# Performance work log

Measured on AMD Instinct MI355X. Metric: run time of the kernel, lower is better.

## Reference

```python
import jax, jax.numpy as jnp
import numpy as np

B, S, D, H = 4, 2048, 1024, 16
HD = D // H
EPS = 1e-5


def setup_inputs() -> dict:
    key = jax.random.key(0)
    ks = jax.random.split(key, 12)
    scale = 1.0 / np.sqrt(D)
    inp = {
        "x": jax.random.normal(ks[0], (B, S, D), dtype=jnp.float32),
        "template_ids": jax.random.randint(ks[1], (B, S), 0, 1000, dtype=jnp.int64)
            if jax.config.jax_enable_x64 else jax.random.randint(ks[1], (B, S), 0, 1000, dtype=jnp.int32),
        "attention_mask": jnp.ones((B, S), dtype=jnp.int32),
        "Wq": jax.random.normal(ks[2], (D, D), dtype=jnp.float32) * scale,
        "bq": jnp.zeros((D,), dtype=jnp.float32),
        "Wk": jax.random.normal(ks[3], (D, D), dtype=jnp.float32) * scale,
        "bk": jnp.zeros((D,), dtype=jnp.float32),
        "Wv": jax.random.normal(ks[4], (D, D), dtype=jnp.float32) * scale,
        "bv": jnp.zeros((D,), dtype=jnp.float32),
        "Wo": jax.random.normal(ks[5], (D, D), dtype=jnp.float32) * scale,
        "bo": jnp.zeros((D,), dtype=jnp.float32),
        "gamma": jnp.ones((D,), dtype=jnp.float32),
        "beta": jnp.zeros((D,), dtype=jnp.float32),
    }
    return inp


def _split_heads(t):
    # [B,S,D] -> [B,H,S,HD]
    return t.reshape(B, S, H, HD).transpose(0, 2, 1, 3)


def reference(x, template_ids, attention_mask, Wq, bq, Wk, bk, Wv, bv, Wo, bo, gamma, beta):
    q = _split_heads(x @ Wq.T + bq)
    k = _split_heads(x @ Wk.T + bk)
    v = _split_heads(x @ Wv.T + bv)
    # [B,H,S,S]
    scores = jnp.einsum("bhqd,bhkd->bhqk", q, k) / jnp.sqrt(jnp.float32(HD))
    mask = attention_mask[:, None, None, :]  # broadcast over heads and query dim
    scores = jnp.where(mask == 0, jnp.float32(-10000.0), scores)
    attn = jax.nn.softmax(scores, axis=-1)  # dropout is identity in eval
    out = jnp.einsum("bhqk,bhkd->bhqd", attn, v)
    out = out.transpose(0, 2, 1, 3).reshape(B, S, D)
    out = out @ Wo.T + bo
    # residual + LayerNorm
    y = x + out
    mu = jnp.mean(y, axis=-1, keepdims=True)
    var = jnp.var(y, axis=-1, keepdims=True)
    return (y - mu) * jax.lax.rsqrt(var + EPS) * gamma + beta
```

## Files before the change

### kernel.cpp

```cpp
#include <hip/hip_runtime.h>

typedef unsigned short u16;
typedef unsigned int u32;
typedef __attribute__((ext_vector_type(8))) short bf16x8;
typedef __attribute__((ext_vector_type(4))) float f32x4;

#define NB 4
#define SS 2048
#define DD 1024
#define NH 16
#define HD 64
#define MM (NB*SS)

struct __align__(16) Pack16 { unsigned int w0, w1, w2, w3; };
union PU { Pack16 p; u16 s[8]; };

__device__ __forceinline__ float b2f(u16 u) {
    union { unsigned int i; float f; } v; v.i = ((unsigned int)u) << 16; return v.f;
}
__device__ __forceinline__ u16 f2b(float f) {
    union { unsigned int i; float f; } v; v.f = f;
    return (u16)((v.i + 0x7FFFu + ((v.i >> 16) & 1u)) >> 16);
}
__device__ __forceinline__ float rdS(const void* p, size_t i, int mode) {
    return mode ? ((const float*)p)[i] : b2f(((const u16*)p)[i]);
}
__device__ __forceinline__ float ex2(float x) { return __builtin_amdgcn_exp2f(x); }
__device__ __forceinline__ u32 cvtpk(float lo, float hi) {
    u32 r;
    asm("v_cvt_pk_bf16_f32 %0, %1, %2" : "=v"(r) : "v"(lo), "v"(hi));
    return r;
}

__device__ __forceinline__ void cp16(const u16* g, u16* l) {
    __builtin_amdgcn_global_load_lds(
        (const __attribute__((address_space(1))) void*)g,
        (__attribute__((address_space(3))) void*)l, 16, 0, 0);
}

__device__ __forceinline__ void pl32swap(u32& a, u32& b) {
    asm volatile("v_permlane32_swap_b32 %0, %1" : "+v"(a), "+v"(b));
}
__device__ __forceinline__ void pl16swap(u32& a, u32& b) {
    asm volatile("v_permlane16_swap_b32 %0, %1" : "+v"(a), "+v"(b));
}

#define QSC 0.1803368801111204f
#define GX ((size_t)MM * DD / 8)
#define GW ((size_t)DD * DD / 8)
#define GTOT (GX + 4 * GW + 512)

__global__ __launch_bounds__(256) void convert_kernel(
    const void* __restrict__ x,
    const void* __restrict__ Wq, const void* __restrict__ Wk,
    const void* __restrict__ Wv, const void* __restrict__ Wo,
    const void* __restrict__ bq, const void* __restrict__ bk,
    const void* __restrict__ bv, const void* __restrict__ bo,
    u16* __restrict__ xb, u16* __restrict__ Wc, u16* __restrict__ Wob,
    u16* __restrict__ bcat, const u32* __restrict__ gamma_w)
{
    const int mode = (gamma_w[0] == 0x3F800000u) ? 1 : 0;
    size_t g = (size_t)blockIdx.x * 256 + threadIdx.x;
    const void* src; u16* dst; size_t off; float sc = 1.0f;
    if (g < GX)               { src = x;  dst = xb;              off = g * 8; }
    else if (g < GX + GW)     { src = Wq; dst = Wc;              off = (g - GX) * 8; sc = QSC; }
    else if (g < GX + 2 * GW) { src = Wk; dst = Wc + (size_t)DD * DD;     off = (g - GX - GW) * 8; }
    else if (g < GX + 3 * GW) { src = Wv; dst = Wc + (size_t)2 * DD * DD; off = (g - GX - 2 * GW) * 8; }
    else if (g < GX + 4 * GW) { src = Wo; dst = Wob;             off = (g - GX - 3 * GW) * 8; }
    else {
        size_t gg = g - (GX + 4 * GW);
        int which = (int)(gg >> 7); off = (gg & 127) * 8;
        src = (which == 0) ? bq : (which == 1) ? bk : (which == 2) ? bv : bo;
        dst = bcat + which * DD;
        if (which == 0) sc = QSC;
    }
    PU o;
    if (mode) {
        const float* s = (const float*)src + off;
        float4 a = ((const float4*)s)[0];
        float4 b = ((const float4*)s)[1];
        o.s[0] = f2b(a.x * sc); o.s[1] = f2b(a.y * sc);
        o.s[2] = f2b(a.z * sc); o.s[3] = f2b(a.w * sc);
        o.s[4] = f2b(b.x * sc); o.s[5] = f2b(b.y * sc);
        o.s[6] = f2b(b.z * sc); o.s[7] = f2b(b.w * sc);
    } else {
        PU in; in.p = *(const Pack16*)((const u16*)src + off);
#pragma unroll
        for (int j = 0; j < 8; j++) o.s[j] = f2b(b2f(in.s[j]) * sc);
    }
    *(Pack16*)(dst + off) = o.p;
}

__global__ __launch_bounds__(256) void gemm_qkv(
    const u16* __restrict__ xb, const u16* __restrict__ Wc, const u16* __restrict__ bcat,
    u16* __restrict__ Q, u16* __restrict__ K, u16* __restrict__ V)
{
    __shared__ __align__(16) u16 sh[2 * 128 * 64];
    u16* As = sh;
    u16* Bs = sh + 128 * 64;

    const int tid  = threadIdx.x;
    const int wv   = tid >> 6;
    const int lane = tid & 63;
    const int wy = wv >> 1, wx = wv & 1;
    const int l15 = lane & 15, quad = lane >> 4;
    const int m0 = blockIdx.x * 128, n0 = blockIdx.y * 128;
    const int srow = lane >> 3;
    const int sw   = ((lane & 7) ^ srow) * 8;
    const int key  = l15 & 7;

    f32x4 acc[4][4];
#pragma unroll
    for (int i = 0; i < 4; i++)
#pragma unroll
        for (int j = 0; j < 4; j++) acc[i][j] = (f32x4){0.f, 0.f, 0.f, 0.f};

    for (int k0 = 0; k0 < DD; k0 += 64) {
#pragma unroll
        for (int c = 0; c < 4; c++) {
            cp16(&xb[(size_t)(m0 + wv * 32 + c * 8 + srow) * DD + k0 + sw],
                 &As[wv * 2048 + c * 512]);
            cp16(&Wc[(size_t)(n0 + wv * 32 + c * 8 + srow) * DD + k0 + sw],
                 &Bs[wv * 2048 + c * 512]);
        }
        __syncthreads();
#pragma unroll
        for (int ks = 0; ks < 2; ks++) {
            bf16x8 a[4], bb[4];
#pragma unroll
            for (int mt = 0; mt < 4; mt++)
                a[mt] = *(const bf16x8*)&As[(wy * 64 + mt * 16 + l15) * 64 +
                                            (((ks << 2) + quad) ^ key) * 8];
#pragma unroll
            for (int nt = 0; nt < 4; nt++)
                bb[nt] = *(const bf16x8*)&Bs[(wx * 64 + nt * 16 + l15) * 64 +
                                             (((ks << 2) + quad) ^ key) * 8];
#pragma unroll
            for (int mt = 0; mt < 4; mt++)
#pragma unroll
                for (int nt = 0; nt < 4; nt++)
                    acc[mt][nt] = __builtin_amdgcn_mfma_f32_16x16x32_bf16(
                        a[mt], bb[nt], acc[mt][nt], 0, 0, 0);
        }
        __syncthreads();
    }

    const int z = n0 >> 10;
    if (z != 2) {
        u16* out = (z == 0) ? Q : K;
#pragma unroll
        for (int nt = 0; nt < 4; nt++) {
            int n_g = n0 + wx * 64 + nt * 16 + l15;
            float bv_ = b2f(bcat[n_g]);
            int nn = n_g & 1023;
            int h = nn >> 6, hd = nn & 63;
#pragma unroll
            for (int mt = 0; mt < 4; mt++) {
#pragma unroll
                for (int r = 0; r < 4; r++) {
                    int m_g = m0 + wy * 64 + mt * 16 + quad * 4 + r;
                    int b = m_g >> 11, s = m_g & (SS - 1);
                    out[(((size_t)(b * NH + h) * SS) + s) * HD + hd] =
                        f2b(acc[mt][nt][r] + bv_);
                }
            }
        }
    } else {
        const int bb_ = m0 >> 11, sbase = m0 & (SS - 1);
#pragma unroll
        for (int ph = 0; ph < 2; ph++) {
            if (wx == ph) {
#pragma unroll
                for (int nt = 0; nt < 4; nt++) {
                    int n_loc = nt * 16 + l15;
                    float bv_ = b2f(bcat[n0 + ph * 64 + n_loc]);
#pragma unroll
                    for (int mt = 0; mt < 4; mt++) {
                        int m = wy * 64 + mt * 16 + quad * 4;
                        uint2 wr;
                        wr.x = (u32)f2b(acc[mt][nt][0] + bv_) |
                               ((u32)f2b(acc[mt][nt][1] + bv_) << 16);
                        wr.y = (u32)f2b(acc[mt][nt][2] + bv_) |
                               ((u32)f2b(acc[mt][nt][3] + bv_) << 16);
                        *(uint2*)&sh[n_loc * 136 + m] = wr;
                    }
                }
            }
            __syncthreads();
            {
                int row = tid >> 2;
                int sg  = tid & 3;
                int n_g = n0 + ph * 64 + row;
                int nn = n_g & 1023;
                int h = nn >> 6, hd = nn & 63;
                u16* dst = &V[(((size_t)(bb_ * NH + h)) * HD + hd) * SS + sbase];
#pragma unroll
                for (int j = 0; j < 4; j++) {
                    int mloc = sg * 32 + j * 8;
                    *(Pack16*)&dst[mloc] = *(const Pack16*)&sh[row * 136 + mloc];
                }
            }
            __syncthreads();
        }
    }
}

__global__ __launch_bounds__(256, 4) void attn_kernel(
    const u16* __restrict__ Q, const u16* __restrict__ K, const u16* __restrict__ V,
    const int* __restrict__ mask, u16* __restrict__ O)
{
    const int bh = blockIdx.y;
    const int b = bh >> 4, h = bh & 15;
    const int q0 = blockIdx.x * 128;
    const u16* Qp  = Q + (size_t)bh * SS * HD;
    const u16* Kp  = K + (size_t)bh * SS * HD;
    const u16* Vtg = V + (size_t)bh * HD * SS;
    const int* mk = mask + b * SS;

    __shared__ __align__(16) u16 Kl[2 * 64 * 64];
    __shared__ __align__(16) u16 Vt[2 * 64 * 64];
    __shared__ int s_anymask;

    const int tid  = threadIdx.x;
    const int w    = tid >> 6;
    const int lane = tid & 63;
    const int l15 = lane & 15, quad = lane >> 4;
    const int srow = lane >> 3;
    const int sw   = ((lane & 7) ^ srow) * 8;
    const int key  = l15 & 7;

    if (tid == 0) s_anymask = 0;
    __syncthreads();
    {
        int local = 0;
#pragma unroll
        for (int i = 0; i < 2; i++) {
            int4 m4 = ((const int4*)mk)[i * 256 + tid];
            if ((m4.x == 0) | (m4.y == 0) | (m4.z == 0) | (m4.w == 0)) local = 1;
        }
        if (local) s_anymask = 1;
    }
    __syncthreads();
    const bool anymask = (s_anymask != 0);

    bf16x8 qf[2][2];
#pragma unroll
    for (int qt = 0; qt < 2; qt++)
#pragma unroll
        for (int ks = 0; ks < 2; ks++)
            qf[qt][ks] = *(const bf16x8*)&Qp[(size_t)(q0 + w * 32 + qt * 16 + l15) * HD +
                                             ks * 32 + quad * 8];

    bf16x8 onesf;
#pragma unroll
    for (int i = 0; i < 8; i++) onesf[i] = (short)0x3F80;

    f32x4 oacc[2][4];
#pragma unroll
    for (int i = 0; i < 2; i++)
#pragma unroll
        for (int j = 0; j < 4; j++) oacc[i][j] = (f32x4){0.f, 0.f, 0.f, 0.f};
    f32x4 sumacc[2];
#pragma unroll
    for (int i = 0; i < 2; i++) sumacc[i] = (f32x4){0.f, 0.f, 0.f, 0.f};

#pragma unroll
    for (int c = 0; c < 2; c++) {
        cp16(&Kp[(size_t)(w * 16 + c * 8 + srow) * HD + sw], &Kl[w * 1024 + c * 512]);
        cp16(&Vtg[(size_t)(w * 16 + c * 8 + srow) * SS + sw], &Vt[w * 1024 + c * 512]);
    }

    for (int it = 0; it < SS / 64; it++) {
        const int kv0 = it * 64;
        const int p = it & 1;
        __syncthreads();

        if (it + 1 < SS / 64) {
            const int kn = kv0 + 64;
#pragma unroll
            for (int c = 0; c < 2; c++) {
                cp16(&Kp[(size_t)(kn + w * 16 + c * 8 + srow) * HD + sw],
                     &Kl[(p ^ 1) * 4096 + w * 1024 + c * 512]);
                cp16(&Vtg[(size_t)(w * 16 + c * 8 + srow) * SS + kn + sw],
                     &Vt[(p ^ 1) * 4096 + w * 1024 + c * 512]);
            }
        }

        f32x4 sacc[4][2];
#pragma unroll
        for (int i = 0; i < 4; i++)
#pragma unroll
            for (int j = 0; j < 2; j++) sacc[i][j] = (f32x4){0.f, 0.f, 0.f, 0.f};
#pragma unroll
        for (int ks = 0; ks < 2; ks++) {
            bf16x8 kf[4];
#pragma unroll
            for (int kvt = 0; kvt < 4; kvt++)
                kf[kvt] = *(const bf16x8*)&Kl[p * 4096 + (kvt * 16 + l15) * 64 +
                                              (((ks << 2) + quad) ^ key) * 8];
            __builtin_amdgcn_s_setprio(1);
#pragma unroll
            for (int kvt = 0; kvt < 4; kvt++)
#pragma unroll
                for (int qt = 0; qt < 2; qt++)
                    sacc[kvt][qt] = __builtin_amdgcn_mfma_f32_16x16x32_bf16(
                        kf[kvt], qf[qt][ks], sacc[kvt][qt], 0, 0, 0);
            __builtin_amdgcn_s_setprio(0);
        }

#pragma unroll
        for (int g = 0; g < 2; g++) {
            union { bf16x8 v; u32 d[4]; } pafq[2];
#pragma unroll
            for (int qt = 0; qt < 2; qt++) {
                u32 pk[2][2];
#pragma unroll
                for (int kk = 0; kk < 2; kk++) {
                    const int kvt = 2 * g + kk;
                    f32x4 vv = sacc[kvt][qt];
                    if (anymask) {
#pragma unroll
                        for (int r = 0; r < 4; r++) {
                            int kv = kv0 + kvt * 16 + quad * 4 + r;
                            if (mk[kv] == 0) vv[r] = -20000.0f;
                        }
                    }
                    pk[kk][0] = cvtpk(ex2(vv[0]), ex2(vv[1]));
                    pk[kk][1] = cvtpk(ex2(vv[2]), ex2(vv[3]));
                }
#pragma unroll
                for (int c = 0; c < 2; c++) {
                    u32 x0 = pk[0][c], x1 = pk[1][c];
                    pl32swap(x0, x1);
                    pl16swap(x0, x1);
                    pafq[qt].d[c]     = x0;
                    pafq[qt].d[2 + c] = x1;
                }
            }
            bf16x8 vf[4];
#pragma unroll
            for (int nt = 0; nt < 4; nt++)
                vf[nt] = *(const bf16x8*)&Vt[p * 4096 + (nt * 16 + l15) * 64 +
                                             (((g << 2) + quad) ^ key) * 8];
            __builtin_amdgcn_s_setprio(1);
#pragma unroll
            for (int qt = 0; qt < 2; qt++) {
#pragma unroll
                for (int nt = 0; nt < 4; nt++)
                    oacc[qt][nt] = __builtin_amdgcn_mfma_f32_16x16x32_bf16(
                        pafq[qt].v, vf[nt], oacc[qt][nt], 0, 0, 0);
                sumacc[qt] = __builtin_amdgcn_mfma_f32_16x16x32_bf16(
                    pafq[qt].v, onesf, sumacc[qt], 0, 0, 0);
            }
            __builtin_amdgcn_s_setprio(0);
        }
    }

#pragma unroll
    for (int qt = 0; qt < 2; qt++) {
#pragma unroll
        for (int r = 0; r < 4; r++) {
            float inv = 1.0f / sumacc[qt][r];
            int row = q0 + w * 32 + qt * 16 + quad * 4 + r;
            size_t base = ((size_t)(b * SS + row)) * DD + h * HD;
#pragma unroll
            for (int nt = 0; nt < 4; nt++)
                O[base + nt * 16 + l15] = f2b(oacc[qt][nt][r] * inv);
        }
    }
}

__global__ __launch_bounds__(256) void gemm_oproj(
    const u16* __restrict__ A, const u16* __restrict__ Wob, const u16* __restrict__ bcat,
    u16* __restrict__ Y0, u16* __restrict__ Y1)
{
    __shared__ __align__(16) u16 As[128 * 64];
    __shared__ __align__(16) u16 Bs[128 * 64];

    const int tid  = threadIdx.x;
    const int wv   = tid >> 6;
    const int lane = tid & 63;
    const int wy = wv >> 1, wx = wv & 1;
    const int l15 = lane & 15, quad = lane >> 4;
    const int m0 = blockIdx.x * 128, n0 = blockIdx.y * 128;
    const int kz = blockIdx.z;
    const int kbase = kz * (DD / 2);
    const int srow = lane >> 3;
    const int sw   = ((lane & 7) ^ srow) * 8;
    const int key  = l15 & 7;

    f32x4 acc[4][4];
#pragma unroll
    for (int i = 0; i < 4; i++)
#pragma unroll
        for (int j = 0; j < 4; j++) acc[i][j] = (f32x4){0.f, 0.f, 0.f, 0.f};

    for (int k0 = 0; k0 < DD / 2; k0 += 64) {
#pragma unroll
        for (int c = 0; c < 4; c++) {
            cp16(&A[(size_t)(m0 + wv * 32 + c * 8 + srow) * DD + kbase + k0 + sw],
                 &As[wv * 2048 + c * 512]);
            cp16(&Wob[(size_t)(n0 + wv * 32 + c * 8 + srow) * DD + kbase + k0 + sw],
                 &Bs[wv * 2048 + c * 512]);
        }
        __syncthreads();
#pragma unroll
        for (int ks = 0; ks < 2; ks++) {
            bf16x8 a[4], bb[4];
#pragma unroll
            for (int mt = 0; mt < 4; mt++)
                a[mt] = *(const bf16x8*)&As[(wy * 64 + mt * 16 + l15) * 64 +
                                            (((ks << 2) + quad) ^ key) * 8];
#pragma unroll
            for (int nt = 0; nt < 4; nt++)
                bb[nt] = *(const bf16x8*)&Bs[(wx * 64 + nt * 16 + l15) * 64 +
                                             (((ks << 2) + quad) ^ key) * 8];
#pragma unroll
            for (int mt = 0; mt < 4; mt++)
#pragma unroll
                for (int nt = 0; nt < 4; nt++)
                    acc[mt][nt] = __builtin_amdgcn_mfma_f32_16x16x32_bf16(
                        a[mt], bb[nt], acc[mt][nt], 0, 0, 0);
        }
        __syncthreads();
    }

    u16* Y = kz ? Y1 : Y0;
#pragma unroll
    for (int nt = 0; nt < 4; nt++) {
        int n_g = n0 + wx * 64 + nt * 16 + l15;
        float bv_ = kz ? 0.f : b2f(bcat[3 * DD + n_g]);
#pragma unroll
        for (int mt = 0; mt < 4; mt++) {
#pragma unroll
            for (int r = 0; r < 4; r++) {
                int m_g = m0 + wy * 64 + mt * 16 + quad * 4 + r;
                Y[(size_t)m_g * DD + n_g] = f2b(acc[mt][nt][r] + bv_);
            }
        }
    }
}

__global__ __launch_bounds__(256) void ln_kernel(
    const u16* __restrict__ Y0p, const u16* __restrict__ Y1p,
    const void* __restrict__ x,
    const void* __restrict__ gamma, const void* __restrict__ beta,
    void* __restrict__ out)
{
    const int mode = (((const u32*)gamma)[0] == 0x3F800000u) ? 1 : 0;
    const int w    = threadIdx.x >> 6;
    const int lane = threadIdx.x & 63;
    const int row  = blockIdx.x * 4 + w;
    const u16* y0 = Y0p + (size_t)row * DD;
    const u16* y1 = Y1p + (size_t)row * DD;

    float vals[16];
    float s = 0.f, sq = 0.f;
#pragma unroll
    for (int i = 0; i < 2; i++) {
        PU d0; d0.p = *(const Pack16*)&y0[i * 512 + lane * 8];
        PU d1; d1.p = *(const Pack16*)&y1[i * 512 + lane * 8];
        if (mode) {
            const float* xp = (const float*)x + (size_t)row * DD + i * 512 + lane * 8;
            float4 xa = ((const float4*)xp)[0];
            float4 xb2 = ((const float4*)xp)[1];
            float xr[8] = {xa.x, xa.y, xa.z, xa.w, xb2.x, xb2.y, xb2.z, xb2.w};
#pragma unroll
            for (int j = 0; j < 8; j++) {
                float f = b2f(d0.s[j]) + b2f(d1.s[j]) + xr[j];
                vals[i * 8 + j] = f;
                s += f; sq += f * f;
            }
        } else {
            const u16* xp = (const u16*)x + (size_t)row * DD + i * 512 + lane * 8;
            PU xd; xd.p = *(const Pack16*)xp;
#pragma unroll
            for (int j = 0; j < 8; j++) {
                float f = b2f(d0.s[j]) + b2f(d1.s[j]) + b2f(xd.s[j]);
                vals[i * 8 + j] = f;
                s += f; sq += f * f;
            }
        }
    }
#pragma unroll
    for (int off = 1; off < 64; off <<= 1) {
        s  += __shfl_xor(s, off);
        sq += __shfl_xor(sq, off);
    }
    float mu  = s * (1.0f / 1024.0f);
    float var = sq * (1.0f / 1024.0f) - mu * mu;
    float rs  = rsqrtf(var + 1e-5f);

#pragma unroll
    for (int i = 0; i < 2; i++) {
        float r8[8];
#pragma unroll
        for (int j = 0; j < 8; j++) {
            int col = i * 512 + lane * 8 + j;
            r8[j] = (vals[i * 8 + j] - mu) * rs * rdS(gamma, col, mode) + rdS(beta, col, mode);
        }
        if (mode) {
            float* of = (float*)out + (size_t)row * DD + i * 512 + lane * 8;
            ((float4*)of)[0] = make_float4(r8[0], r8[1], r8[2], r8[3]);
            ((float4*)of)[1] = make_float4(r8[4], r8[5], r8[6], r8[7]);
        } else {
            PU ob;
#pragma unroll
            for (int j = 0; j < 8; j++) ob.s[j] = f2b(r8[j]);
            *(Pack16*)((u16*)out + (size_t)row * DD + i * 512 + lane * 8) = ob.p;
        }
    }
}

extern "C" void kernel_launch(void* const* d_in, const int* in_sizes, int n_in,
                              void* d_out, int out_size, void* d_ws, size_t ws_size,
                              hipStream_t stream)
{
    const void* x     = d_in[0];
    const int* mask   = (const int*)d_in[2];
    const void* Wq    = d_in[3];
    const void* bq    = d_in[4];
    const void* Wk    = d_in[5];
    const void* bk    = d_in[6];
    const void* Wv    = d_in[7];
    const void* bv    = d_in[8];
    const void* Wo    = d_in[9];
    const void* bo    = d_in[10];
    const void* gamma = d_in[11];
    const void* beta  = d_in[12];

    const size_t n = (size_t)MM * DD;
    u16* xb   = (u16*)((char*)d_ws + 256);
    u16* Wc   = xb + n;
    u16* Wob  = Wc + (size_t)3 * DD * DD;
    u16* bcat = Wob + (size_t)DD * DD;
    u16* Qb   = bcat + 4096;
    u16* Kb   = Qb + n;
    u16* Vb   = Kb + n;
    u16* Ab   = Vb + n;

    convert_kernel<<<(unsigned)(GTOT / 256), 256, 0, stream>>>(
        x, Wq, Wk, Wv, Wo, bq, bk, bv, bo, xb, Wc, Wob, bcat, (const u32*)gamma);
    gemm_qkv<<<dim3(MM / 128, 3 * DD / 128), 256, 0, stream>>>(xb, Wc, bcat, Qb, Kb, Vb);
    attn_kernel<<<dim3(SS / 128, NB * NH), 256, 0, stream>>>(Qb, Kb, Vb, mask, Ab);
    gemm_oproj<<<dim3(MM / 128, DD / 128, 2), 256, 0, stream>>>(Ab, Wob, bcat, Qb, Kb);
    ln_kernel<<<MM / 4, 256, 0, stream>>>(Qb, Kb, x, gamma, beta, d_out);
}
```

Measured before the change: 326.4 us.

## Remap attention grid for XCD-aware K/V locality and batch softmax packing

Switches the attention launch to a 1D grid of 1024 blocks and remaps each block index so that consecutive blocks, which round-robin across the 8 XCDs, land on the same (batch, head) per XCD. The aim is for K/V tiles to be reused in each XCD's L2. It also restructures the P computation so that exp and bf16 packing run for all four KV tiles before any PV MFMAs are issued, which gives the scheduler more independent work. The cost is higher register pressure from holding every packed P fragment at once.

```diff
diff --git a/kernel.cpp b/kernel.cpp
--- a/kernel.cpp
+++ b/kernel.cpp
@@ -209,9 +209,11 @@
     const u16* __restrict__ Q, const u16* __restrict__ K, const u16* __restrict__ V,
     const int* __restrict__ mask, u16* __restrict__ O)
 {
-    const int bh = blockIdx.y;
+    const int lin  = blockIdx.x;
+    const int slot = lin >> 3;
+    const int bh   = (lin & 7) * 8 + (slot >> 4);
     const int b = bh >> 4, h = bh & 15;
-    const int q0 = blockIdx.x * 128;
+    const int q0 = (slot & 15) * 128;
     const u16* Qp  = Q + (size_t)bh * SS * HD;
     const u16* Kp  = K + (size_t)bh * SS * HD;
     const u16* Vtg = V + (size_t)bh * HD * SS;
@@ -308,49 +310,53 @@
             __builtin_amdgcn_s_setprio(0);
         }
 
-#pragma unroll
-        for (int g = 0; g < 2; g++) {
-            union { bf16x8 v; u32 d[4]; } pafq[2];
-#pragma unroll
-            for (int qt = 0; qt < 2; qt++) {
-                u32 pk[2][2];
-#pragma unroll
-                for (int kk = 0; kk < 2; kk++) {
-                    const int kvt = 2 * g + kk;
-                    f32x4 vv = sacc[kvt][qt];
-                    if (anymask) {
-#pragma unroll
-                        for (int r = 0; r < 4; r++) {
-                            int kv = kv0 + kvt * 16 + quad * 4 + r;
-                            if (mk[kv] == 0) vv[r] = -20000.0f;
-                        }
+        union { bf16x8 v; u32 d[4]; } paf[2][2];
+#pragma unroll
+        for (int qt = 0; qt < 2; qt++) {
+            u32 pk[4][2];
+#pragma unroll
+            for (int kvt = 0; kvt < 4; kvt++) {
+                f32x4 vv = sacc[kvt][qt];
+                if (anymask) {
+#pragma unroll
+                    for (int r = 0; r < 4; r++) {
+                        int kv = kv0 + kvt * 16 + quad * 4 + r;
+                        if (mk[kv] == 0) vv[r] = -20000.0f;
                     }
-                    pk[kk][0] = cvtpk(ex2(vv[0]), ex2(vv[1]));
-                    pk[kk][1] = cvtpk(ex2(vv[2]), ex2(vv[3]));
                 }
+                pk[kvt][0] = cvtpk(ex2(vv[0]), ex2(vv[1]));
+                pk[kvt][1] = cvtpk(ex2(vv[2]), ex2(vv[3]));
+            }
+#pragma unroll
+            for (int ks2 = 0; ks2 < 2; ks2++) {
 #pragma unroll
                 for (int c = 0; c < 2; c++) {
-                    u32 x0 = pk[0][c], x1 = pk[1][c];
+                    u32 x0 = pk[ks2 * 2 + 0][c];
+                    u32 x1 = pk[ks2 * 2 + 1][c];
                     pl32swap(x0, x1);
                     pl16swap(x0, x1);
-                    pafq[qt].d[c]     = x0;
-                    pafq[qt].d[2 + c] = x1;
+                    paf[qt][ks2].d[c]     = x0;
+                    paf[qt][ks2].d[2 + c] = x1;
                 }
             }
+        }
+
+#pragma unroll
+        for (int ks2 = 0; ks2 < 2; ks2++) {
             bf16x8 vf[4];
 #pragma unroll
             for (int nt = 0; nt < 4; nt++)
                 vf[nt] = *(const bf16x8*)&Vt[p * 4096 + (nt * 16 + l15) * 64 +
-                                             (((g << 2) + quad) ^ key) * 8];
+                                             (((ks2 << 2) + quad) ^ key) * 8];
             __builtin_amdgcn_s_setprio(1);
 #pragma unroll
             for (int qt = 0; qt < 2; qt++) {
 #pragma unroll
                 for (int nt = 0; nt < 4; nt++)
                     oacc[qt][nt] = __builtin_amdgcn_mfma_f32_16x16x32_bf16(
-                        pafq[qt].v, vf[nt], oacc[qt][nt], 0, 0, 0);
+                        paf[qt][ks2].v, vf[nt], oacc[qt][nt], 0, 0, 0);
                 sumacc[qt] = __builtin_amdgcn_mfma_f32_16x16x32_bf16(
-                    pafq[qt].v, onesf, sumacc[qt], 0, 0, 0);
+                    paf[qt][ks2].v, onesf, sumacc[qt], 0, 0, 0);
             }
             __builtin_amdgcn_s_setprio(0);
         }
@@ -542,7 +548,7 @@
     convert_kernel<<<(unsigned)(GTOT / 256), 256, 0, stream>>>(
         x, Wq, Wk, Wv, Wo, bq, bk, bv, bo, xb, Wc, Wob, bcat, (const u32*)gamma);
     gemm_qkv<<<dim3(MM / 128, 3 * DD / 128), 256, 0, stream>>>(xb, Wc, bcat, Qb, Kb, Vb);
-    attn_kernel<<<dim3(SS / 128, NB * NH), 256, 0, stream>>>(Qb, Kb, Vb, mask, Ab);
+    attn_kernel<<<1024, 256, 0, stream>>>(Qb, Kb, Vb, mask, Ab);
     gemm_oproj<<<dim3(MM / 128, DD / 128, 2), 256, 0, stream>>>(Ab, Wob, bcat, Qb, Kb);
     ln_kernel<<<MM / 4, 256, 0, stream>>>(Qb, Kb, x, gamma, beta, d_out);
 }
```

Measured after the change: 317.6 us. -2.7%, faster.
